# Optimization experiments

Hardware: AMD Instinct MI355X
Metric: run time of the kernel (lower is better)

The kernel has to match this reference:

```python
import jax, jax.numpy as jnp
import numpy as np

IMG_H, IMG_W = 800, 1216   # input image size (stride-32 backbone)
FH, FW = 25, 38            # feature map spatial dims
C = 2048                   # feature channels (100352 = 2048*7*7)
N_BOXES = 2000             # RPN proposals
N_KEEP = 8                 # hard-coded `for i in range(0, 8)` in source
NMS_THRESH = 0.6


def _pairwise_iou(box, boxes):
    # box [4] vs boxes [N,4], corner (x1,y1,x2,y2) format, torchvision convention
    ix1 = jnp.maximum(box[0], boxes[:, 0])
    iy1 = jnp.maximum(box[1], boxes[:, 1])
    ix2 = jnp.minimum(box[2], boxes[:, 2])
    iy2 = jnp.minimum(box[3], boxes[:, 3])
    inter = jnp.clip(ix2 - ix1, 0.0) * jnp.clip(iy2 - iy1, 0.0)
    a1 = (box[2] - box[0]) * (box[3] - box[1])
    a2 = (boxes[:, 2] - boxes[:, 0]) * (boxes[:, 3] - boxes[:, 1])
    return inter / (a1 + a2 - inter)


def _adaptive_maxpool_roi(feat, x, y, w, h):
    # feat [C,FH,FW]; pool window rows [y, y+h), cols [x, x+w) down to 7x7
    # PyTorch AdaptiveMaxPool2d: cell i covers [floor(i*h/7), ceil((i+1)*h/7))
    i = jnp.arange(7)
    r0 = y + (i * h) // 7
    r1 = y + ((i + 1) * h + 6) // 7
    c0 = x + (i * w) // 7
    c1 = x + ((i + 1) * w + 6) // 7
    rows = jnp.arange(feat.shape[1])
    cols = jnp.arange(feat.shape[2])
    rmask = (rows[None, :] >= r0[:, None]) & (rows[None, :] < r1[:, None])  # [7,FH]
    cmask = (cols[None, :] >= c0[:, None]) & (cols[None, :] < c1[:, None])  # [7,FW]
    # row reduce: [C,7,FW], then col reduce: [C,7,7]
    t = jnp.where(rmask[None, :, :, None], feat[:, None, :, :], -jnp.inf).max(axis=2)
    out = jnp.where(cmask[None, None, :, :], t[:, :, None, :], -jnp.inf).max(axis=3)
    return out


def setup_inputs() -> dict:
    key = jax.random.key(0)
    ks = jax.random.split(key, 12)
    feat_map = jax.random.normal(ks[0], (1, C, FH, FW), dtype=jnp.float32)
    # proposals fully inside the image (so index_inside keeps them)
    x1 = jax.random.uniform(ks[1], (N_BOXES,), minval=0.0, maxval=IMG_W - 256.0)
    y1 = jax.random.uniform(ks[2], (N_BOXES,), minval=0.0, maxval=IMG_H - 256.0)
    bw = jax.random.uniform(ks[3], (N_BOXES,), minval=16.0, maxval=256.0)
    bh = jax.random.uniform(ks[4], (N_BOXES,), minval=16.0, maxval=256.0)
    rois = jnp.stack([x1, y1, x1 + bw, y1 + bh], axis=1).astype(jnp.float32)
    scores = jax.random.uniform(ks[5], (N_BOXES, 2), dtype=jnp.float32)
    s = 0.01  # nn.init.normal_(w, 0, 0.01)
    return {
        "feat_map": feat_map,
        "rois": rois,
        "scores": scores,
        "w1": jax.random.normal(ks[6], (4096, 100352), dtype=jnp.float32) * s,
        "b1": jnp.zeros((4096,), jnp.float32),
        "w2": jax.random.normal(ks[7], (4096, 4096), dtype=jnp.float32) * s,
        "b2": jnp.zeros((4096,), jnp.float32),
        "wc": jax.random.normal(ks[8], (81, 4096), dtype=jnp.float32) * s,
        "bc": jnp.zeros((81,), jnp.float32),
        "wl": jax.random.normal(ks[9], (324, 4096), dtype=jnp.float32) * s,
        "bl": jnp.zeros((324,), jnp.float32),
    }


def reference(feat_map, rois, scores, w1, b1, w2, b2, wc, bc, wl, bl):
    feat = feat_map[0]  # [C,FH,FW]
    # index_inside filter
    valid = (rois[:, 0] >= 0) & (rois[:, 1] >= 0) & (rois[:, 2] <= IMG_W) & (rois[:, 3] <= IMG_H)
    fg = scores[:, 1]
    # greedy NMS: first N_KEEP survivors at IoU 0.6 == torchvision.ops.nms(...)[:8]
    alive = valid
    sels = []
    for _ in range(N_KEEP):
        m = jnp.where(alive, fg, -jnp.inf)
        s = jnp.argmax(m)
        sels.append(s)
        iou = _pairwise_iou(rois[s], rois)
        alive = alive & (iou <= NMS_THRESH)
    sels = jnp.stack(sels)
    b = rois[sels] / 32.0  # [8,4]
    # faithful to source: x,y,w,h = int(x+0.5), int(y+0.5), int(w+1), int(h+1)
    x = jnp.floor(b[:, 0] + 0.5).astype(jnp.int32)
    y = jnp.floor(b[:, 1] + 0.5).astype(jnp.int32)
    w = jnp.floor(b[:, 2] + 1.0).astype(jnp.int32)
    h = jnp.floor(b[:, 3] + 1.0).astype(jnp.int32)
    bad = (x < 0) | (x >= FW) | (y < 0) | (y >= FH) | (w < 1) | (x + w > FW) | (h < 1) | (y + h > FH)
    # fallback: pool the entire feature map (roi = feat_map[0])
    x = jnp.where(bad, 0, x)
    y = jnp.where(bad, 0, y)
    w = jnp.where(bad, FW, w)
    h = jnp.where(bad, FH, h)
    pooled = jax.vmap(lambda xx, yy, ww, hh: _adaptive_maxpool_roi(feat, xx, yy, ww, hh))(x, y, w, h)  # [8,C,7,7]
    flat = pooled.reshape(N_KEEP, -1)  # [8,100352]
    o = flat @ w1.T + b1   # no activation in the original
    o = o @ w2.T + b2
    roi_scores = o @ wc.T + bc  # [8,81]
    roi_locs = o @ wl.T + bl    # [8,324]
    return jnp.concatenate([roi_scores, roi_locs], axis=-1)  # [8,405]
```

## Files before the change

### kernel.cpp

```cpp
#include <hip/hip_runtime.h>
#include <cstddef>
#include <math.h>

typedef float v4 __attribute__((ext_vector_type(4)));

#define IMG_H 800
#define IMG_W 1216
#define FH 25
#define FWW 38
#define NBOX 2000
#define NKEEP 8
#define D1 100352
#define K1 4096
#define NSLICE 16
#define DPS (D1/NSLICE)

__global__ __launch_bounds__(256) void nms_sel_kernel(const float* __restrict__ rois,
                                                      const float* __restrict__ scores,
                                                      int* __restrict__ roi_out) {
    __shared__ float4 s_box[NBOX];
    __shared__ float  s_fg[NBOX];
    __shared__ float  red_v[256];
    __shared__ int    red_i[256];
    __shared__ int    s_sels[NKEEP];
    const int tid = threadIdx.x;

    for (int i = tid; i < NBOX; i += 256) {
        float x1 = rois[i*4+0], y1 = rois[i*4+1], x2 = rois[i*4+2], y2 = rois[i*4+3];
        s_box[i] = make_float4(x1, y1, x2, y2);
        bool valid = (x1 >= 0.f) && (y1 >= 0.f) && (x2 <= (float)IMG_W) && (y2 <= (float)IMG_H);
        s_fg[i] = valid ? scores[i*2+1] : -INFINITY;
    }
    __syncthreads();

    for (int it = 0; it < NKEEP; ++it) {
        float bv = -INFINITY; int bi = NBOX;
        for (int i = tid; i < NBOX; i += 256) {
            float v = s_fg[i];
            if (v > bv || (v == bv && i < bi)) { bv = v; bi = i; }
        }
        red_v[tid] = bv; red_i[tid] = bi;
        __syncthreads();
        for (int off = 128; off > 0; off >>= 1) {
            if (tid < off) {
                float v = red_v[tid+off]; int ii = red_i[tid+off];
                if (v > red_v[tid] || (v == red_v[tid] && ii < red_i[tid])) {
                    red_v[tid] = v; red_i[tid] = ii;
                }
            }
            __syncthreads();
        }
        int s = red_i[0];
        if (s >= NBOX) s = 0;
        if (tid == 0) s_sels[it] = s;

        float4 bs = s_box[s];
        float a1 = (bs.z - bs.x) * (bs.w - bs.y);
        for (int i = tid; i < NBOX; i += 256) {
            float4 b = s_box[i];
            float ix1 = fmaxf(bs.x, b.x), iy1 = fmaxf(bs.y, b.y);
            float ix2 = fminf(bs.z, b.z), iy2 = fminf(bs.w, b.w);
            float inter = fmaxf(ix2 - ix1, 0.f) * fmaxf(iy2 - iy1, 0.f);
            float a2 = (b.z - b.x) * (b.w - b.y);
            float iou = inter / (a1 + a2 - inter);
            if (!(iou <= 0.6f)) s_fg[i] = -INFINITY;
        }
        __syncthreads();
    }

    if (tid < NKEEP) {
        int s = s_sels[tid];
        float4 b = s_box[s];
        int x = (int)floorf(b.x / 32.0f + 0.5f);
        int y = (int)floorf(b.y / 32.0f + 0.5f);
        int w = (int)floorf(b.z / 32.0f + 1.0f);
        int h = (int)floorf(b.w / 32.0f + 1.0f);
        bool bad = (x < 0) || (x >= FWW) || (y < 0) || (y >= FH) ||
                   (w < 1) || (x + w > FWW) || (h < 1) || (y + h > FH);
        if (bad) { x = 0; y = 0; w = FWW; h = FH; }
        roi_out[tid*4+0] = x; roi_out[tid*4+1] = y;
        roi_out[tid*4+2] = w; roi_out[tid*4+3] = h;
    }
}

__global__ __launch_bounds__(256) void roi_pool_kernel(const float* __restrict__ feat,
                                                       const int* __restrict__ roi_out,
                                                       float* __restrict__ pooled) {
    int idx = blockIdx.x * 256 + threadIdx.x;
    if (idx >= NKEEP * D1) return;
    int r    = idx / D1;
    int rem  = idx - r * D1;
    int c    = rem / 49;
    int cell = rem - c * 49;
    int i = cell / 7;
    int j = cell - i * 7;
    int x = roi_out[r*4+0], y = roi_out[r*4+1], w = roi_out[r*4+2], h = roi_out[r*4+3];
    int r0 = y + (i * h) / 7;
    int r1 = y + ((i + 1) * h + 6) / 7;
    int c0 = x + (j * w) / 7;
    int c1 = x + ((j + 1) * w + 6) / 7;
    const float* fc = feat + (size_t)c * (FH * FWW);
    float m = -INFINITY;
    for (int rr = r0; rr < r1; ++rr) {
        const float* fr = fc + rr * FWW;
        for (int cc2 = c0; cc2 < c1; ++cc2) m = fmaxf(m, fr[cc2]);
    }
    pooled[idx] = m;
}

__global__ __launch_bounds__(256) void init_bias8_kernel(const float* __restrict__ b,
                                                         float* __restrict__ o, int K) {
    int i = blockIdx.x * 256 + threadIdx.x;
    if (i < NKEEP * K) o[i] = b[i & (K - 1)];
}

__global__ __launch_bounds__(256) void fc1_kernel(const float* __restrict__ w1,
                                                  const float* __restrict__ flat,
                                                  float* __restrict__ o1) {
    const int kb = blockIdx.x >> 4;
    const int ds = blockIdx.x & 15;
    const int tid = threadIdx.x;
    const int kq = tid >> 4;
    const int dl = tid & 15;
    const int k0 = kb * 64 + kq * 4;
    const int dbase = ds * DPS + dl * 4;

    const float* wp = w1 + (size_t)k0 * D1 + dbase;
    const float* fp = flat + dbase;

    float acc[4][8];
    #pragma unroll
    for (int a = 0; a < 4; ++a)
        #pragma unroll
        for (int n = 0; n < 8; ++n) acc[a][n] = 0.f;

    v4 wa[4];
    #pragma unroll
    for (int a = 0; a < 4; ++a) wa[a] = *(const v4*)(wp + (size_t)a * D1);

    for (int itn = 0; itn < DPS / 64; ++itn) {
        const int off  = itn * 64;
        const int offn = (itn < DPS / 64 - 1) ? off + 64 : off;

        v4 fv[8];
        #pragma unroll
        for (int n = 0; n < 8; ++n) fv[n] = *(const v4*)(fp + (size_t)n * D1 + off);

        v4 wb[4];
        #pragma unroll
        for (int a = 0; a < 4; ++a) wb[a] = *(const v4*)(wp + (size_t)a * D1 + offn);

        #pragma unroll
        for (int n = 0; n < 8; ++n) {
            acc[0][n] += wa[0][0]*fv[n][0] + wa[0][1]*fv[n][1] + wa[0][2]*fv[n][2] + wa[0][3]*fv[n][3];
            acc[1][n] += wa[1][0]*fv[n][0] + wa[1][1]*fv[n][1] + wa[1][2]*fv[n][2] + wa[1][3]*fv[n][3];
            acc[2][n] += wa[2][0]*fv[n][0] + wa[2][1]*fv[n][1] + wa[2][2]*fv[n][2] + wa[2][3]*fv[n][3];
            acc[3][n] += wa[3][0]*fv[n][0] + wa[3][1]*fv[n][1] + wa[3][2]*fv[n][2] + wa[3][3]*fv[n][3];
        }

        #pragma unroll
        for (int a = 0; a < 4; ++a) wa[a] = wb[a];
    }

    #pragma unroll
    for (int a = 0; a < 4; ++a) {
        #pragma unroll
        for (int n = 0; n < 8; ++n) {
            float v = acc[a][n];
            v += __shfl_xor(v, 1);
            v += __shfl_xor(v, 2);
            v += __shfl_xor(v, 4);
            v += __shfl_xor(v, 8);
            if (dl == 0) atomicAdd(&o1[n * K1 + k0 + a], v);
        }
    }
}

__global__ __launch_bounds__(256) void fc2_kernel(const float* __restrict__ w2,
                                                  const float* __restrict__ o1,
                                                  const float* __restrict__ b2,
                                                  float* __restrict__ o2) {
    int gw   = (blockIdx.x * 256 + threadIdx.x) >> 6;
    int lane = threadIdx.x & 63;
    if (gw >= K1) return;
    const float4* wr = (const float4*)(w2 + (size_t)gw * K1);
    const float4* fo = (const float4*)o1;
    float acc[8];
    #pragma unroll
    for (int n = 0; n < 8; ++n) acc[n] = 0.f;
    for (int itn = 0; itn < K1 / 256; ++itn) {
        float4 wv = wr[itn * 64 + lane];
        #pragma unroll
        for (int n = 0; n < 8; ++n) {
            float4 f = fo[n * (K1/4) + itn * 64 + lane];
            acc[n] += wv.x*f.x + wv.y*f.y + wv.z*f.z + wv.w*f.w;
        }
    }
    #pragma unroll
    for (int n = 0; n < 8; ++n) {
        float v = acc[n];
        #pragma unroll
        for (int m = 32; m >= 1; m >>= 1) v += __shfl_xor(v, m);
        if (lane == 0) o2[n * K1 + gw] = v + b2[gw];
    }
}

__global__ __launch_bounds__(256) void fc3_kernel(const float* __restrict__ wc,
                                                  const float* __restrict__ bc,
                                                  const float* __restrict__ wl,
                                                  const float* __restrict__ bl,
                                                  const float* __restrict__ o2,
                                                  float* __restrict__ out) {
    int gw   = (blockIdx.x * 256 + threadIdx.x) >> 6;
    int lane = threadIdx.x & 63;
    if (gw >= 405) return;
    const float* wrow; float bias;
    if (gw < 81) { wrow = wc + (size_t)gw * K1;        bias = bc[gw]; }
    else         { wrow = wl + (size_t)(gw - 81) * K1; bias = bl[gw - 81]; }
    const float4* wr = (const float4*)wrow;
    const float4* fo = (const float4*)o2;
    float acc[8];
    #pragma unroll
    for (int n = 0; n < 8; ++n) acc[n] = 0.f;
    for (int itn = 0; itn < K1 / 256; ++itn) {
        float4 wv = wr[itn * 64 + lane];
        #pragma unroll
        for (int n = 0; n < 8; ++n) {
            float4 f = fo[n * (K1/4) + itn * 64 + lane];
            acc[n] += wv.x*f.x + wv.y*f.y + wv.z*f.z + wv.w*f.w;
        }
    }
    #pragma unroll
    for (int n = 0; n < 8; ++n) {
        float v = acc[n];
        #pragma unroll
        for (int m = 32; m >= 1; m >>= 1) v += __shfl_xor(v, m);
        if (lane == 0) out[n * 405 + gw] = v + bias;
    }
}

extern "C" void kernel_launch(void* const* d_in, const int* in_sizes, int n_in,
                              void* d_out, int out_size, void* d_ws, size_t ws_size,
                              hipStream_t stream) {
    const float* feat   = (const float*)d_in[0];
    const float* rois   = (const float*)d_in[1];
    const float* scores = (const float*)d_in[2];
    const float* w1     = (const float*)d_in[3];
    const float* b1     = (const float*)d_in[4];
    const float* w2     = (const float*)d_in[5];
    const float* b2     = (const float*)d_in[6];
    const float* wc     = (const float*)d_in[7];
    const float* bc     = (const float*)d_in[8];
    const float* wl     = (const float*)d_in[9];
    const float* bl     = (const float*)d_in[10];
    float* out = (float*)d_out;

    int*   roi_out = (int*)d_ws;
    float* pooled  = (float*)d_ws + 256;
    float* o1      = pooled + (size_t)NKEEP * D1;
    float* o2      = o1 + NKEEP * K1;

    nms_sel_kernel<<<1, 256, 0, stream>>>(rois, scores, roi_out);
    roi_pool_kernel<<<(NKEEP * D1 + 255) / 256, 256, 0, stream>>>(feat, roi_out, pooled);
    init_bias8_kernel<<<(NKEEP * K1 + 255) / 256, 256, 0, stream>>>(b1, o1, K1);
    fc1_kernel<<<64 * NSLICE, 256, 0, stream>>>(w1, pooled, o1);
    fc2_kernel<<<K1 / 4, 256, 0, stream>>>(w2, o1, b2, o2);
    fc3_kernel<<<(405 * 64 + 255) / 256, 256, 0, stream>>>(wc, bc, wl, bl, o2, out);
}
```

Before: 405.2 us.

## Raise occupancy in FC kernels and widen NMS block to 1024 threads

The fc1 kernel now gives each thread 2 output rows instead of 4, doubles the grid, drops the software prefetch of weights, and sets launch bounds asking for 8 waves per SIMD. The goal is to cut register pressure and hide memory latency on the 1.6 GB weight stream. The fc2 kernel splits each row's dot product across two waves with a shared-memory combine and unrolls the loop. This also aims at higher occupancy and more loads in flight. The NMS selection kernel uses 1024 threads so each thread handles fewer boxes, at the cost of a deeper reduction.

```diff
diff --git a/kernel.cpp b/kernel.cpp
--- a/kernel.cpp
+++ b/kernel.cpp
@@ -15,17 +15,17 @@
 #define NSLICE 16
 #define DPS (D1/NSLICE)
 
-__global__ __launch_bounds__(256) void nms_sel_kernel(const float* __restrict__ rois,
-                                                      const float* __restrict__ scores,
-                                                      int* __restrict__ roi_out) {
+__global__ __launch_bounds__(1024) void nms_sel_kernel(const float* __restrict__ rois,
+                                                       const float* __restrict__ scores,
+                                                       int* __restrict__ roi_out) {
     __shared__ float4 s_box[NBOX];
     __shared__ float  s_fg[NBOX];
-    __shared__ float  red_v[256];
-    __shared__ int    red_i[256];
+    __shared__ float  red_v[1024];
+    __shared__ int    red_i[1024];
     __shared__ int    s_sels[NKEEP];
     const int tid = threadIdx.x;
 
-    for (int i = tid; i < NBOX; i += 256) {
+    for (int i = tid; i < NBOX; i += 1024) {
         float x1 = rois[i*4+0], y1 = rois[i*4+1], x2 = rois[i*4+2], y2 = rois[i*4+3];
         s_box[i] = make_float4(x1, y1, x2, y2);
         bool valid = (x1 >= 0.f) && (y1 >= 0.f) && (x2 <= (float)IMG_W) && (y2 <= (float)IMG_H);
@@ -35,13 +35,13 @@
 
     for (int it = 0; it < NKEEP; ++it) {
         float bv = -INFINITY; int bi = NBOX;
-        for (int i = tid; i < NBOX; i += 256) {
+        for (int i = tid; i < NBOX; i += 1024) {
             float v = s_fg[i];
             if (v > bv || (v == bv && i < bi)) { bv = v; bi = i; }
         }
         red_v[tid] = bv; red_i[tid] = bi;
         __syncthreads();
-        for (int off = 128; off > 0; off >>= 1) {
+        for (int off = 512; off > 0; off >>= 1) {
             if (tid < off) {
                 float v = red_v[tid+off]; int ii = red_i[tid+off];
                 if (v > red_v[tid] || (v == red_v[tid] && ii < red_i[tid])) {
@@ -56,7 +56,7 @@
 
         float4 bs = s_box[s];
         float a1 = (bs.z - bs.x) * (bs.w - bs.y);
-        for (int i = tid; i < NBOX; i += 256) {
+        for (int i = tid; i < NBOX; i += 1024) {
             float4 b = s_box[i];
             float ix1 = fmaxf(bs.x, b.x), iy1 = fmaxf(bs.y, b.y);
             float ix2 = fminf(bs.z, b.z), iy2 = fminf(bs.w, b.w);
@@ -114,56 +114,54 @@
     if (i < NKEEP * K) o[i] = b[i & (K - 1)];
 }
 
-__global__ __launch_bounds__(256) void fc1_kernel(const float* __restrict__ w1,
-                                                  const float* __restrict__ flat,
-                                                  float* __restrict__ o1) {
+__global__ __launch_bounds__(256, 8) void fc1_kernel(const float* __restrict__ w1,
+                                                     const float* __restrict__ flat,
+                                                     float* __restrict__ o1) {
     const int kb = blockIdx.x >> 4;
     const int ds = blockIdx.x & 15;
     const int tid = threadIdx.x;
     const int kq = tid >> 4;
     const int dl = tid & 15;
-    const int k0 = kb * 64 + kq * 4;
+    const int k0 = kb * 32 + kq * 2;
     const int dbase = ds * DPS + dl * 4;
 
     const float* wp = w1 + (size_t)k0 * D1 + dbase;
     const float* fp = flat + dbase;
 
-    float acc[4][8];
-    #pragma unroll
-    for (int a = 0; a < 4; ++a)
+    float acc[2][8];
+    #pragma unroll
+    for (int a = 0; a < 2; ++a)
         #pragma unroll
         for (int n = 0; n < 8; ++n) acc[a][n] = 0.f;
 
-    v4 wa[4];
-    #pragma unroll
-    for (int a = 0; a < 4; ++a) wa[a] = *(const v4*)(wp + (size_t)a * D1);
-
     for (int itn = 0; itn < DPS / 64; ++itn) {
-        const int off  = itn * 64;
-        const int offn = (itn < DPS / 64 - 1) ? off + 64 : off;
-
-        v4 fv[8];
-        #pragma unroll
-        for (int n = 0; n < 8; ++n) fv[n] = *(const v4*)(fp + (size_t)n * D1 + off);
-
-        v4 wb[4];
-        #pragma unroll
-        for (int a = 0; a < 4; ++a) wb[a] = *(const v4*)(wp + (size_t)a * D1 + offn);
-
-        #pragma unroll
-        for (int n = 0; n < 8; ++n) {
-            acc[0][n] += wa[0][0]*fv[n][0] + wa[0][1]*fv[n][1] + wa[0][2]*fv[n][2] + wa[0][3]*fv[n][3];
-            acc[1][n] += wa[1][0]*fv[n][0] + wa[1][1]*fv[n][1] + wa[1][2]*fv[n][2] + wa[1][3]*fv[n][3];
-            acc[2][n] += wa[2][0]*fv[n][0] + wa[2][1]*fv[n][1] + wa[2][2]*fv[n][2] + wa[2][3]*fv[n][3];
-            acc[3][n] += wa[3][0]*fv[n][0] + wa[3][1]*fv[n][1] + wa[3][2]*fv[n][2] + wa[3][3]*fv[n][3];
-        }
-
-        #pragma unroll
-        for (int a = 0; a < 4; ++a) wa[a] = wb[a];
-    }
-
-    #pragma unroll
-    for (int a = 0; a < 4; ++a) {
+        const int off = itn * 64;
+        v4 wv0 = *(const v4*)(wp + off);
+        v4 wv1 = *(const v4*)(wp + (size_t)D1 + off);
+        {
+            v4 fv[4];
+            #pragma unroll
+            for (int n = 0; n < 4; ++n) fv[n] = *(const v4*)(fp + (size_t)n * D1 + off);
+            #pragma unroll
+            for (int n = 0; n < 4; ++n) {
+                acc[0][n] += wv0[0]*fv[n][0] + wv0[1]*fv[n][1] + wv0[2]*fv[n][2] + wv0[3]*fv[n][3];
+                acc[1][n] += wv1[0]*fv[n][0] + wv1[1]*fv[n][1] + wv1[2]*fv[n][2] + wv1[3]*fv[n][3];
+            }
+        }
+        {
+            v4 fv[4];
+            #pragma unroll
+            for (int n = 0; n < 4; ++n) fv[n] = *(const v4*)(fp + (size_t)(n + 4) * D1 + off);
+            #pragma unroll
+            for (int n = 0; n < 4; ++n) {
+                acc[0][n+4] += wv0[0]*fv[n][0] + wv0[1]*fv[n][1] + wv0[2]*fv[n][2] + wv0[3]*fv[n][3];
+                acc[1][n+4] += wv1[0]*fv[n][0] + wv1[1]*fv[n][1] + wv1[2]*fv[n][2] + wv1[3]*fv[n][3];
+            }
+        }
+    }
+
+    #pragma unroll
+    for (int a = 0; a < 2; ++a) {
         #pragma unroll
         for (int n = 0; n < 8; ++n) {
             float v = acc[a][n];
@@ -176,32 +174,49 @@
     }
 }
 
-__global__ __launch_bounds__(256) void fc2_kernel(const float* __restrict__ w2,
-                                                  const float* __restrict__ o1,
-                                                  const float* __restrict__ b2,
-                                                  float* __restrict__ o2) {
-    int gw   = (blockIdx.x * 256 + threadIdx.x) >> 6;
-    int lane = threadIdx.x & 63;
-    if (gw >= K1) return;
-    const float4* wr = (const float4*)(w2 + (size_t)gw * K1);
-    const float4* fo = (const float4*)o1;
+__global__ __launch_bounds__(256, 8) void fc2_kernel(const float* __restrict__ w2,
+                                                     const float* __restrict__ o1,
+                                                     const float* __restrict__ b2,
+                                                     float* __restrict__ o2) {
+    __shared__ float red[4][8];
+    const int tid  = threadIdx.x;
+    const int wid  = tid >> 6;
+    const int lane = tid & 63;
+    const int row  = blockIdx.x * 2 + (wid >> 1);
+    const int half = wid & 1;
+    const int base = half * (K1 / 2);
+
+    const float* wr = w2 + (size_t)row * K1 + base + lane * 4;
+    const float* fo = o1 + base + lane * 4;
+
     float acc[8];
     #pragma unroll
     for (int n = 0; n < 8; ++n) acc[n] = 0.f;
-    for (int itn = 0; itn < K1 / 256; ++itn) {
-        float4 wv = wr[itn * 64 + lane];
+    #pragma unroll
+    for (int i = 0; i < 8; ++i) {
+        const int off = i * 256;
+        v4 wv = *(const v4*)(wr + off);
         #pragma unroll
         for (int n = 0; n < 8; ++n) {
-            float4 f = fo[n * (K1/4) + itn * 64 + lane];
-            acc[n] += wv.x*f.x + wv.y*f.y + wv.z*f.z + wv.w*f.w;
+            v4 f = *(const v4*)(fo + (size_t)n * K1 + off);
+            acc[n] += wv[0]*f[0] + wv[1]*f[1] + wv[2]*f[2] + wv[3]*f[3];
         }
     }
     #pragma unroll
     for (int n = 0; n < 8; ++n) {
         float v = acc[n];
-        #pragma unroll
-        for (int m = 32; m >= 1; m >>= 1) v += __shfl_xor(v, m);
-        if (lane == 0) o2[n * K1 + gw] = v + b2[gw];
+        v += __shfl_xor(v, 1);  v += __shfl_xor(v, 2);
+        v += __shfl_xor(v, 4);  v += __shfl_xor(v, 8);
+        v += __shfl_xor(v, 16); v += __shfl_xor(v, 32);
+        if (lane == 0) red[wid][n] = v;
+    }
+    __syncthreads();
+    if (tid < 16) {
+        int p = tid >> 3;
+        int n = tid & 7;
+        int r = blockIdx.x * 2 + p;
+        float v = red[p*2][n] + red[p*2+1][n];
+        o2[n * K1 + r] = v + b2[r];
     }
 }
 
@@ -260,10 +275,10 @@
     float* o1      = pooled + (size_t)NKEEP * D1;
     float* o2      = o1 + NKEEP * K1;
 
-    nms_sel_kernel<<<1, 256, 0, stream>>>(rois, scores, roi_out);
+    nms_sel_kernel<<<1, 1024, 0, stream>>>(rois, scores, roi_out);
     roi_pool_kernel<<<(NKEEP * D1 + 255) / 256, 256, 0, stream>>>(feat, roi_out, pooled);
     init_bias8_kernel<<<(NKEEP * K1 + 255) / 256, 256, 0, stream>>>(b1, o1, K1);
-    fc1_kernel<<<64 * NSLICE, 256, 0, stream>>>(w1, pooled, o1);
-    fc2_kernel<<<K1 / 4, 256, 0, stream>>>(w2, o1, b2, o2);
+    fc1_kernel<<<128 * NSLICE, 256, 0, stream>>>(w1, pooled, o1);
+    fc2_kernel<<<K1 / 2, 256, 0, stream>>>(w2, o1, b2, o2);
     fc3_kernel<<<(405 * 64 + 255) / 256, 256, 0, stream>>>(wc, bc, wl, bl, o2, out);
 }
```

Measured after the change: 859.5 us. 112% more time.

## Split fc1 rows between original kernel and new wave-per-row-group kernel

Applied to the files above, without the earlier changes.

Halves the grid of the original fc1 kernel so it covers only the first 2048 output rows, and adds a new kernel for rows 2048-4095. In the new kernel each wave handles four weight rows over a 3584-wide slice of the input dimension, loading weights in two interleaved chunks and reducing across the full wave before an atomic add. The aim is to improve streaming of the large fc1 weight matrix through a different access pattern and more blocks. The two kernels run back to back, so any gain depends on the new kernel's bandwidth, and the halved original grid is assumed to map onto the first 2048 rows.

```diff
diff --git a/kernel.cpp b/kernel.cpp
--- a/kernel.cpp
+++ b/kernel.cpp
@@ -176,6 +176,80 @@
     }
 }
 
+__global__ __launch_bounds__(256) void fc1_waverow_kernel(const float* __restrict__ w1,
+                                                          const float* __restrict__ flat,
+                                                          const float* __restrict__ b1,
+                                                          float* __restrict__ o1) {
+    const int bid = blockIdx.x;
+    const int rg  = bid / 28;
+    const int ds  = bid - rg * 28;
+    const int wid  = threadIdx.x >> 6;
+    const int lane = threadIdx.x & 63;
+    const int row0  = 2048 + rg * 16 + wid * 4;
+    const int dbase = ds * 3584;
+
+    const float* wp = w1 + (size_t)row0 * D1 + dbase + lane * 4;
+    const float* fp = flat + dbase + lane * 4;
+
+    float acc[4][8];
+    #pragma unroll
+    for (int a = 0; a < 4; ++a)
+        #pragma unroll
+        for (int n = 0; n < 8; ++n) acc[a][n] = 0.f;
+
+    for (int t2 = 0; t2 < 7; ++t2) {
+        const int off0 = t2 * 512;
+        const int off1 = off0 + 256;
+
+        v4 wA[4], wB[4];
+        #pragma unroll
+        for (int a = 0; a < 4; ++a) {
+            wA[a] = *(const v4*)(wp + (size_t)a * D1 + off0);
+            wB[a] = *(const v4*)(wp + (size_t)a * D1 + off1);
+        }
+
+        {
+            v4 fv[8];
+            #pragma unroll
+            for (int n = 0; n < 8; ++n) fv[n] = *(const v4*)(fp + (size_t)n * D1 + off0);
+            #pragma unroll
+            for (int n = 0; n < 8; ++n) {
+                acc[0][n] += wA[0][0]*fv[n][0] + wA[0][1]*fv[n][1] + wA[0][2]*fv[n][2] + wA[0][3]*fv[n][3];
+                acc[1][n] += wA[1][0]*fv[n][0] + wA[1][1]*fv[n][1] + wA[1][2]*fv[n][2] + wA[1][3]*fv[n][3];
+                acc[2][n] += wA[2][0]*fv[n][0] + wA[2][1]*fv[n][1] + wA[2][2]*fv[n][2] + wA[2][3]*fv[n][3];
+                acc[3][n] += wA[3][0]*fv[n][0] + wA[3][1]*fv[n][1] + wA[3][2]*fv[n][2] + wA[3][3]*fv[n][3];
+            }
+        }
+        {
+            v4 fv[8];
+            #pragma unroll
+            for (int n = 0; n < 8; ++n) fv[n] = *(const v4*)(fp + (size_t)n * D1 + off1);
+            #pragma unroll
+            for (int n = 0; n < 8; ++n) {
+                acc[0][n] += wB[0][0]*fv[n][0] + wB[0][1]*fv[n][1] + wB[0][2]*fv[n][2] + wB[0][3]*fv[n][3];
+                acc[1][n] += wB[1][0]*fv[n][0] + wB[1][1]*fv[n][1] + wB[1][2]*fv[n][2] + wB[1][3]*fv[n][3];
+                acc[2][n] += wB[2][0]*fv[n][0] + wB[2][1]*fv[n][1] + wB[2][2]*fv[n][2] + wB[2][3]*fv[n][3];
+                acc[3][n] += wB[3][0]*fv[n][0] + wB[3][1]*fv[n][1] + wB[3][2]*fv[n][2] + wB[3][3]*fv[n][3];
+            }
+        }
+    }
+
+    #pragma unroll
+    for (int a = 0; a < 4; ++a) {
+        #pragma unroll
+        for (int n = 0; n < 8; ++n) {
+            float v = acc[a][n];
+            v += __shfl_xor(v, 1);
+            v += __shfl_xor(v, 2);
+            v += __shfl_xor(v, 4);
+            v += __shfl_xor(v, 8);
+            v += __shfl_xor(v, 16);
+            v += __shfl_xor(v, 32);
+            if (lane == 0) atomicAdd(&o1[n * K1 + row0 + a], v);
+        }
+    }
+}
+
 __global__ __launch_bounds__(256) void fc2_kernel(const float* __restrict__ w2,
                                                   const float* __restrict__ o1,
                                                   const float* __restrict__ b2,
@@ -263,7 +337,8 @@
     nms_sel_kernel<<<1, 256, 0, stream>>>(rois, scores, roi_out);
     roi_pool_kernel<<<(NKEEP * D1 + 255) / 256, 256, 0, stream>>>(feat, roi_out, pooled);
     init_bias8_kernel<<<(NKEEP * K1 + 255) / 256, 256, 0, stream>>>(b1, o1, K1);
-    fc1_kernel<<<64 * NSLICE, 256, 0, stream>>>(w1, pooled, o1);
+    fc1_kernel<<<32 * NSLICE, 256, 0, stream>>>(w1, pooled, o1);
+    fc1_waverow_kernel<<<128 * 28, 256, 0, stream>>>(w1, pooled, b1, o1);
     fc2_kernel<<<K1 / 4, 256, 0, stream>>>(w2, o1, b2, o2);
     fc3_kernel<<<(405 * 64 + 255) / 256, 256, 0, stream>>>(wc, bc, wl, bl, o2, out);
 }
```

After: 593.4 us. 1.46x slower.
